# Kernel tuning notes

Hardware: AMD Instinct MI355X
Metric: run time of the kernel (lower is better)

Reference implementation:

```python
import jax, jax.numpy as jnp
import numpy as np

B, N, C = 128, 8732, 21  # batch, SSD priors, VOC classes (incl. background)
EPS = 1e-7


def setup_inputs() -> dict:
    key = jax.random.key(0)
    k1, k2, k3 = jax.random.split(key, 3)
    return {
        "lam": jnp.float32(0.7),
        "conf": jax.random.uniform(k1, (B, N, C), dtype=jnp.float32),
        "conf_shuffle": jax.random.uniform(k2, (B, N, C), dtype=jnp.float32),
        "conf_interpolation": jax.random.uniform(k3, (B, N, C), dtype=jnp.float32),
    }


def reference(lam, conf, conf_shuffle, conf_interpolation):
    half = conf.shape[0] // 2
    # swap the two halves of the shuffled batch
    conf_temp = jnp.concatenate([conf_shuffle[half:], conf_shuffle[:half]], axis=0)

    # foreground mask: max class score beats background score, on both sides
    left_mask = jnp.max(conf[..., 1:], axis=-1) > conf[..., 0]
    right_mask = jnp.max(conf_temp[..., 1:], axis=-1) > conf_temp[..., 0]
    mask = (left_mask & right_mask).astype(conf.dtype)  # [B, N]

    mixed = lam * conf + (1.0 - lam) * conf_temp + EPS
    inter = conf_interpolation + EPS

    sg = jax.lax.stop_gradient
    # KLDivLoss(log_input, target) = target * (log(target) - log_input), summed over classes
    inter_t = sg(inter)
    kl_a = jnp.sum(inter_t * (jnp.log(inter_t) - jnp.log(mixed)), axis=-1)  # [B, N]
    mixed_t = sg(mixed)
    kl_b = jnp.sum(mixed_t * (jnp.log(mixed_t) - jnp.log(inter)), axis=-1)  # [B, N]

    cnt = jnp.sum(mask)
    # masked mean over selected (b, n) samples; 0 if mask empty
    loss = jnp.sum((kl_a + kl_b) * mask) / jnp.maximum(cnt, 1.0)
    return jnp.where(cnt > 0, loss / 2.0, jnp.float32(0.0))
```

## Files before the change

kernel.cpp:

```cpp
#include <hip/hip_runtime.h>


#define EPS 1e-7f

constexpr int B = 128;
constexpr int N = 8732;
constexpr int C = 21;
constexpr int ROWS = B * N;
constexpr int TILE = 256;
constexpr int BLOCK = 256;
constexpr int GRID = ROWS / TILE;
constexpr int TILE_ELEMS = TILE * C;
constexpr int TILE_F4 = TILE_ELEMS / 4;
constexpr int BATCH_F4 = (N * C) / 4;

__global__ __launch_bounds__(BLOCK) void isd_main_kernel(
    const float* __restrict__ lam_p,
    const float* __restrict__ conf,
    const float* __restrict__ csh,
    const float* __restrict__ cin,
    double* __restrict__ partials)
{
    __shared__ float s_conf[TILE_ELEMS];
    __shared__ float s_csh [TILE_ELEMS];
    __shared__ float s_cin [TILE_ELEMS];

    const int tid = threadIdx.x;
    const int tileF4base = blockIdx.x * TILE_F4;

    const float4* conf4 = (const float4*)conf;
    const float4* csh4  = (const float4*)csh;
    const float4* cin4  = (const float4*)cin;

    for (int k = tid; k < TILE_F4; k += BLOCK) {
        const int G = tileF4base + k;
        ((float4*)s_conf)[k] = conf4[G];
        ((float4*)s_cin )[k] = cin4[G];
        const int b  = G / BATCH_F4;
        const int G2 = G + ((b ^ 64) - b) * BATCH_F4;
        ((float4*)s_csh)[k] = csh4[G2];
    }
    __syncthreads();

    const float lam = lam_p[0];
    const float oml = 1.0f - lam;

    const float* pc = s_conf + tid * C;
    const float* pt = s_csh  + tid * C;
    const float* pi = s_cin  + tid * C;

    float c0 = 0.0f, t0 = 0.0f;
    float cmax = -1e30f, tmax = -1e30f;
    float kl = 0.0f;

    #pragma unroll
    for (int c = 0; c < C; ++c) {
        const float cv = pc[c];
        const float tv = pt[c];
        const float iv = pi[c] + EPS;
        const float mv = fmaf(lam, cv, oml * tv) + EPS;
        kl += (iv - mv) * (__logf(iv) - __logf(mv));
        if (c == 0) { c0 = cv; t0 = tv; }
        else        { cmax = fmaxf(cmax, cv); tmax = fmaxf(tmax, tv); }
    }

    const float msk = ((cmax > c0) && (tmax > t0)) ? 1.0f : 0.0f;
    float sum = kl * msk;
    float cnt = msk;

    #pragma unroll
    for (int off = 32; off > 0; off >>= 1) {
        sum += __shfl_down(sum, off, 64);
        cnt += __shfl_down(cnt, off, 64);
    }

    __shared__ float r_sum[BLOCK / 64];
    __shared__ float r_cnt[BLOCK / 64];
    const int wave = tid >> 6;
    const int lane = tid & 63;
    if (lane == 0) { r_sum[wave] = sum; r_cnt[wave] = cnt; }
    __syncthreads();

    if (tid == 0) {
        double bs = 0.0, bc = 0.0;
        #pragma unroll
        for (int w = 0; w < BLOCK / 64; ++w) { bs += (double)r_sum[w]; bc += (double)r_cnt[w]; }
        partials[2 * blockIdx.x + 0] = bs;
        partials[2 * blockIdx.x + 1] = bc;
    }
}

__global__ __launch_bounds__(256) void isd_final_kernel(
    const double* __restrict__ partials,
    float* __restrict__ out)
{
    double s = 0.0, c = 0.0;
    for (int i = threadIdx.x; i < GRID; i += 256) {
        s += partials[2 * i + 0];
        c += partials[2 * i + 1];
    }
    #pragma unroll
    for (int off = 32; off > 0; off >>= 1) {
        s += __shfl_down(s, off, 64);
        c += __shfl_down(c, off, 64);
    }
    __shared__ double ss[4], sc[4];
    const int wave = threadIdx.x >> 6;
    const int lane = threadIdx.x & 63;
    if (lane == 0) { ss[wave] = s; sc[wave] = c; }
    __syncthreads();
    if (threadIdx.x == 0) {
        const double S  = ss[0] + ss[1] + ss[2] + ss[3];
        const double Cc = sc[0] + sc[1] + sc[2] + sc[3];
        out[0] = (Cc > 0.0) ? (float)(S / fmax(Cc, 1.0) * 0.5) : 0.0f;
    }
}

extern "C" void kernel_launch(void* const* d_in, const int* in_sizes, int n_in,
                              void* d_out, int out_size, void* d_ws, size_t ws_size,
                              hipStream_t stream) {
    const float* lam  = (const float*)d_in[0];
    const float* conf = (const float*)d_in[1];
    const float* csh  = (const float*)d_in[2];
    const float* cin  = (const float*)d_in[3];
    float* out = (float*)d_out;
    double* partials = (double*)d_ws;

    isd_main_kernel<<<GRID, BLOCK, 0, stream>>>(lam, conf, csh, cin, partials);
    isd_final_kernel<<<1, 256, 0, stream>>>(partials, out);
}
```

Measured before the change: 274.3 us.

## Load rows directly into registers with float4, four rows per thread

Drops the shared-memory staging tile. Each thread now handles 4 consecutive rows (21 float4 per tensor) loaded straight from global memory into registers, which removes the LDS round trip and the barrier. Per-thread loads are strided by 84 floats, so coalescing across lanes gets worse. Register use goes up, and the shuffle reduction is now done in double precision.

```diff
diff --git a/kernel.cpp b/kernel.cpp
--- a/kernel.cpp
+++ b/kernel.cpp
@@ -7,86 +7,96 @@
 constexpr int N = 8732;
 constexpr int C = 21;
 constexpr int ROWS = B * N;
-constexpr int TILE = 256;
+constexpr int RPT = 4;
+constexpr int GROUPS = ROWS / RPT;
 constexpr int BLOCK = 256;
-constexpr int GRID = ROWS / TILE;
-constexpr int TILE_ELEMS = TILE * C;
-constexpr int TILE_F4 = TILE_ELEMS / 4;
+constexpr int GRID = (GROUPS + BLOCK - 1) / BLOCK;
+constexpr int F4_PER_GROUP = RPT * C / 4;
 constexpr int BATCH_F4 = (N * C) / 4;
+constexpr int GROUPS_PER_BATCH = N / RPT;
 
-__global__ __launch_bounds__(BLOCK) void isd_main_kernel(
+__global__ __launch_bounds__(BLOCK, 4) void isd_main_kernel(
     const float* __restrict__ lam_p,
     const float* __restrict__ conf,
     const float* __restrict__ csh,
     const float* __restrict__ cin,
     double* __restrict__ partials)
 {
-    __shared__ float s_conf[TILE_ELEMS];
-    __shared__ float s_csh [TILE_ELEMS];
-    __shared__ float s_cin [TILE_ELEMS];
+    const int gid = blockIdx.x * BLOCK + threadIdx.x;
 
-    const int tid = threadIdx.x;
-    const int tileF4base = blockIdx.x * TILE_F4;
+    double bs = 0.0, bc = 0.0;
 
-    const float4* conf4 = (const float4*)conf;
-    const float4* csh4  = (const float4*)csh;
-    const float4* cin4  = (const float4*)cin;
+    if (gid < GROUPS) {
+        const float4* conf4 = (const float4*)conf;
+        const float4* csh4  = (const float4*)csh;
+        const float4* cin4  = (const float4*)cin;
 
-    for (int k = tid; k < TILE_F4; k += BLOCK) {
-        const int G = tileF4base + k;
-        ((float4*)s_conf)[k] = conf4[G];
-        ((float4*)s_cin )[k] = cin4[G];
-        const int b  = G / BATCH_F4;
-        const int G2 = G + ((b ^ 64) - b) * BATCH_F4;
-        ((float4*)s_csh)[k] = csh4[G2];
+        const int b     = gid / GROUPS_PER_BATCH;
+        const int base  = gid * F4_PER_GROUP;
+        const int base2 = base + ((b ^ 64) - b) * BATCH_F4;
+
+        const float lam = lam_p[0];
+        const float oml = 1.0f - lam;
+
+        float kl[RPT]   = {0.0f, 0.0f, 0.0f, 0.0f};
+        float c0[RPT], t0[RPT], cmax[RPT], tmax[RPT];
+
+        #pragma unroll
+        for (int j = 0; j < F4_PER_GROUP; ++j) {
+            const float4 cf = conf4[base  + j];
+            const float4 tf = csh4 [base2 + j];
+            const float4 vf = cin4 [base  + j];
+            const float* cp = (const float*)&cf;
+            const float* tp = (const float*)&tf;
+            const float* ip = (const float*)&vf;
+            #pragma unroll
+            for (int e = 0; e < 4; ++e) {
+                const int idx = 4 * j + e;
+                const int r   = idx / C;
+                const int c   = idx % C;
+                const float cv = cp[e];
+                const float tv = tp[e];
+                const float iv = ip[e] + EPS;
+                const float mv = fmaf(lam, cv, oml * tv) + EPS;
+                kl[r] += (iv - mv) * (__logf(iv) - __logf(mv));
+                if (c == 0) {
+                    c0[r] = cv; t0[r] = tv;
+                    cmax[r] = -1e30f; tmax[r] = -1e30f;
+                } else {
+                    cmax[r] = fmaxf(cmax[r], cv);
+                    tmax[r] = fmaxf(tmax[r], tv);
+                }
+            }
+        }
+
+        #pragma unroll
+        for (int r = 0; r < RPT; ++r) {
+            if ((cmax[r] > c0[r]) && (tmax[r] > t0[r])) {
+                bs += (double)kl[r];
+                bc += 1.0;
+            }
+        }
     }
-    __syncthreads();
-
-    const float lam = lam_p[0];
-    const float oml = 1.0f - lam;
-
-    const float* pc = s_conf + tid * C;
-    const float* pt = s_csh  + tid * C;
-    const float* pi = s_cin  + tid * C;
-
-    float c0 = 0.0f, t0 = 0.0f;
-    float cmax = -1e30f, tmax = -1e30f;
-    float kl = 0.0f;
-
-    #pragma unroll
-    for (int c = 0; c < C; ++c) {
-        const float cv = pc[c];
-        const float tv = pt[c];
-        const float iv = pi[c] + EPS;
-        const float mv = fmaf(lam, cv, oml * tv) + EPS;
-        kl += (iv - mv) * (__logf(iv) - __logf(mv));
-        if (c == 0) { c0 = cv; t0 = tv; }
-        else        { cmax = fmaxf(cmax, cv); tmax = fmaxf(tmax, tv); }
-    }
-
-    const float msk = ((cmax > c0) && (tmax > t0)) ? 1.0f : 0.0f;
-    float sum = kl * msk;
-    float cnt = msk;
 
     #pragma unroll
     for (int off = 32; off > 0; off >>= 1) {
-        sum += __shfl_down(sum, off, 64);
-        cnt += __shfl_down(cnt, off, 64);
+        bs += __shfl_down(bs, off, 64);
+        bc += __shfl_down(bc, off, 64);
     }
 
-    __shared__ float r_sum[BLOCK / 64];
-    __shared__ float r_cnt[BLOCK / 64];
-    const int wave = tid >> 6;
-    const int lane = tid & 63;
-    if (lane == 0) { r_sum[wave] = sum; r_cnt[wave] = cnt; }
+    __shared__ double r_sum[BLOCK / 64];
+    __shared__ double r_cnt[BLOCK / 64];
+    const int wave = threadIdx.x >> 6;
+    const int lane = threadIdx.x & 63;
+    if (lane == 0) { r_sum[wave] = bs; r_cnt[wave] = bc; }
     __syncthreads();
 
-    if (tid == 0) {
-        double bs = 0.0, bc = 0.0;
+    if (threadIdx.x == 0) {
+        double s = 0.0, c = 0.0;
         #pragma unroll
-        for (int w = 0; w < BLOCK / 64; ++w) { bs += (double)r_sum[w]; bc += (double)r_cnt[w]; }
-        partials[2 * blockIdx.x + 0] = bs;
-        partials[2 * blockIdx.x + 1] = bc;
+        for (int w = 0; w < BLOCK / 64; ++w) { s += r_sum[w]; c += r_cnt[w]; }
+        partials[2 * blockIdx.x + 0] = s;
+        partials[2 * blockIdx.x + 1] = c;
     }
 }
 
```

New measurement: 394.2 us. 1.44x slower.
